# Optimization experiments

Measured on AMD Instinct MI355X. Metric: run time of the kernel, lower is better.

The kernel has to match this reference:

```python
import jax, jax.numpy as jnp
import numpy as np

B, L, D = 4, 1024, 512
H, DH = 8, 64
E = 65536  # total subgraph node entries
BN_EPS = 1e-5


def setup_inputs() -> dict:
    key = jax.random.key(0)
    ks = jax.random.split(key, 16)
    x = jax.random.normal(ks[0], (B, L, D), dtype=jnp.float32)
    lattice = jax.random.normal(ks[1], (B, 6), dtype=jnp.float32)  # unused (cond_dim=0)
    B_graph = jax.random.normal(ks[2], (B, L, L), dtype=jnp.float32) * 0.02
    N = B * L
    subgraph_node_index = jax.random.randint(ks[3], (E,), 0, N, dtype=jnp.int32)
    subgraph_indicator = jnp.sort(jax.random.randint(ks[4], (E,), 0, N, dtype=jnp.int32))
    attn_mask = jnp.triu(jnp.ones((L, L), dtype=bool), k=1)  # True = masked (causal)
    s = 0.02
    # Linear weights stored as [in, out]
    Wq = jax.random.normal(ks[5], (D, H * DH), jnp.float32) * s
    Wk = jax.random.normal(ks[6], (D, H * DH), jnp.float32) * s
    Wv = jax.random.normal(ks[7], (D, H * DH), jnp.float32) * s
    Wo = jax.random.normal(ks[8], (H * DH, D), jnp.float32) * s
    bq = jnp.zeros((H * DH,), jnp.float32)
    bk = jnp.zeros((H * DH,), jnp.float32)
    bv = jnp.zeros((H * DH,), jnp.float32)
    bo = jnp.zeros((D,), jnp.float32)
    Wmp = jax.random.normal(ks[9], (D, D), jnp.float32) * s
    bmp = jnp.zeros((D,), jnp.float32)
    bn_gamma = jnp.ones((2 * D,), jnp.float32)
    bn_beta = jnp.zeros((2 * D,), jnp.float32)
    Wex = jax.random.normal(ks[10], (2 * D, D), jnp.float32) * s
    bex = jnp.zeros((D,), jnp.float32)
    struct_scale = jnp.zeros((1,), jnp.float32) + 0.1  # nonzero so bias path is exercised
    return dict(x=x, lattice=lattice, B_graph=B_graph,
                subgraph_node_index=subgraph_node_index,
                subgraph_indicator=subgraph_indicator, attn_mask=attn_mask,
                Wq=Wq, bq=bq, Wk=Wk, bk=bk, Wv=Wv, bv=bv, Wo=Wo, bo=bo,
                Wmp=Wmp, bmp=bmp, bn_gamma=bn_gamma, bn_beta=bn_beta,
                Wex=Wex, bex=bex, struct_scale=struct_scale)


def _extractor(x_flat, sub_idx, sub_ind, Wmp, bmp, bn_gamma, bn_beta, Wex, bex):
    N = x_flat.shape[0]
    x_sub = x_flat[sub_idx]                       # [E, D]
    h = x_sub + (x_sub @ Wmp + bmp)               # 1 message-passing layer (residual)
    # scatter_mean over subgraph_indicator, dim_size=N
    sums = jax.ops.segment_sum(h, sub_ind, num_segments=N)
    cnt = jax.ops.segment_sum(jnp.ones((h.shape[0],), h.dtype), sub_ind, num_segments=N)
    h_pool = sums / jnp.maximum(cnt, 1.0)[:, None]
    out = jnp.concatenate([x_flat, h_pool], axis=-1)  # [N, 2D]
    # BatchNorm1d (training-mode batch stats)
    mu = jnp.mean(out, axis=0)
    var = jnp.var(out, axis=0)
    out = (out - mu) * jax.lax.rsqrt(var + BN_EPS) * bn_gamma + bn_beta
    return out @ Wex + bex                        # [N, D]


def reference(x, lattice, B_graph, subgraph_node_index, subgraph_indicator, attn_mask,
              Wq, bq, Wk, bk, Wv, bv, Wo, bo, Wmp, bmp, bn_gamma, bn_beta,
              Wex, bex, struct_scale):
    Bb, Ll, Dd = x.shape
    scale = 1.0 / np.sqrt(DH).astype(np.float32)
    q = (x @ Wq + bq).reshape(Bb, Ll, H, DH).transpose(0, 2, 1, 3)
    k = (x @ Wk + bk).reshape(Bb, Ll, H, DH).transpose(0, 2, 1, 3)
    v = (x @ Wv + bv).reshape(Bb, Ll, H, DH).transpose(0, 2, 1, 3)
    scores = jnp.einsum('bhqd,bhkd->bhqk', q, k) * scale
    # structural bias from GNN extractor
    x_flat = x.reshape(Bb * Ll, Dd)
    ex = _extractor(x_flat, subgraph_node_index, subgraph_indicator,
                    Wmp, bmp, bn_gamma, bn_beta, Wex, bex)
    x_struct = ex.reshape(Bb, Ll, Dd)
    K = jnp.einsum('bqd,bkd->bqk', x_struct, x_struct) / np.sqrt(Dd).astype(np.float32)
    scores = scores + struct_scale[0] * K[:, None]
    scores = scores + B_graph[:, None]
    mask = attn_mask[None, None]                  # (1,1,L,L), True = masked
    scores = jnp.where(mask, jnp.float32(-10000.0), scores)
    attn = jax.nn.softmax(scores.astype(jnp.float32), axis=-1).astype(scores.dtype)
    # dropout is identity (eval / p effectively 0)
    out = jnp.einsum('bhqk,bhkd->bhqd', attn, v)
    out = out.transpose(0, 2, 1, 3).reshape(Bb, Ll, H * DH)
    out = out @ Wo + bo
    return out, attn
```

## Files before the change

kernel.cpp:

```cpp
#include <hip/hip_runtime.h>
#include <math.h>

#define BB 4
#define LL 1024
#define DD 512
#define HH 8
#define DHH 64
#define EE 65536
#define NNODES 4096
#define HD 512
#define TWO_D 1024

typedef short bf16x8 __attribute__((ext_vector_type(8)));
typedef short short4v __attribute__((ext_vector_type(4)));
typedef float f32x4 __attribute__((ext_vector_type(4)));
typedef unsigned int u32;
#define GL_AS __attribute__((address_space(1)))
#define LDS_AS __attribute__((address_space(3)))

__device__ __forceinline__ short f2bf(float f) {
  u32 u = __builtin_bit_cast(u32, f);
  u = (u + 0x7fffu + ((u >> 16) & 1u)) >> 16;
  return (short)u;
}
__device__ __forceinline__ float b2f(short s) {
  u32 u = ((u32)(unsigned short)s) << 16;
  return __builtin_bit_cast(float, u);
}
__device__ __forceinline__ void gload_lds16(const short* g, short* l) {
  __builtin_amdgcn_global_load_lds((GL_AS const u32*)g, (LDS_AS u32*)l, 16, 0, 0);
}

template <int ROWS>
__device__ __forceinline__ void stage32(const short* g, int lda, short* lds, int tid) {
  const int w = tid >> 6, l = tid & 63;
#pragma unroll
  for (int rep = 0; rep < ROWS / 64; ++rep) {
    const int rbase = rep * 64 + w * 16;
    gload_lds16(g + (size_t)(rbase + (l >> 2)) * lda + (l & 3) * 8, lds + rbase * 32);
  }
}
__device__ __forceinline__ void stage64x128(const short* g, int lda, short* lds, int tid) {
  const int w = tid >> 6, l = tid & 63;
#pragma unroll
  for (int rep = 0; rep < 4; ++rep) {
    const int rbase = rep * 32 + w * 8;
    gload_lds16(g + (size_t)(rbase + (l >> 3)) * lda + (l & 7) * 8, lds + rbase * 64);
  }
}

template <int MREP, int NREP>
__device__ __forceinline__ void mfma_step(const short* As, const short* Bs, int lds_ld, int kofs,
                                          f32x4 (&acc)[MREP][NREP], int wr, int wc, int l) {
  bf16x8 a[MREP], b[NREP];
#pragma unroll
  for (int mi = 0; mi < MREP; ++mi) {
    const int row = wr * (MREP * 16) + mi * 16 + (l & 15);
    a[mi] = *(const bf16x8*)(As + row * lds_ld + kofs + ((l >> 4) << 3));
  }
#pragma unroll
  for (int ni = 0; ni < NREP; ++ni) {
    const int row = wc * (NREP * 16) + ni * 16 + (l & 15);
    b[ni] = *(const bf16x8*)(Bs + row * lds_ld + kofs + ((l >> 4) << 3));
  }
#pragma unroll
  for (int mi = 0; mi < MREP; ++mi)
#pragma unroll
    for (int ni = 0; ni < NREP; ++ni)
      acc[mi][ni] = __builtin_amdgcn_mfma_f32_16x16x32_bf16(a[mi], b[ni], acc[mi][ni], 0, 0, 0);
}

__global__ __launch_bounds__(256) void k_cast_x(const float* __restrict__ x, short* __restrict__ xb) {
  const int i = (blockIdx.x * 256 + threadIdx.x) * 8;
  float4 f0 = *(const float4*)(x + i), f1 = *(const float4*)(x + i + 4);
  bf16x8 s;
  s[0] = f2bf(f0.x); s[1] = f2bf(f0.y); s[2] = f2bf(f0.z); s[3] = f2bf(f0.w);
  s[4] = f2bf(f1.x); s[5] = f2bf(f1.y); s[6] = f2bf(f1.z); s[7] = f2bf(f1.w);
  *(bf16x8*)(xb + i) = s;
}

__global__ __launch_bounds__(256) void k_tcast(const float* __restrict__ W, short* __restrict__ out,
                                               int K, int N) {
  __shared__ float t[32][33];
  const int k0 = blockIdx.y * 32, n0 = blockIdx.x * 32;
  const int tx = threadIdx.x, ty = threadIdx.y;
#pragma unroll
  for (int i = 0; i < 4; ++i)
    t[ty + 8 * i][tx] = W[(size_t)(k0 + ty + 8 * i) * N + n0 + tx];
  __syncthreads();
#pragma unroll
  for (int i = 0; i < 4; ++i)
    out[(size_t)(n0 + ty + 8 * i) * K + k0 + tx] = f2bf(t[tx][ty + 8 * i]);
}

__global__ __launch_bounds__(256) void k_pack_bias(const float* bq, const float* bk,
                                                   const float* bv, const float* bmp,
                                                   float* __restrict__ bcat) {
  const int i = blockIdx.x * 256 + threadIdx.x;
  const float* src = (i < 512) ? bq : (i < 1024) ? bk : (i < 1536) ? bv : bmp;
  bcat[i] = src[i & 511];
}

__global__ __launch_bounds__(256) void k_gemm_qkvg(const short* __restrict__ A,
                                                   const short* __restrict__ Bw,
                                                   const float* __restrict__ bcat,
                                                   const float* __restrict__ x,
                                                   short* __restrict__ qT, short* __restrict__ kT,
                                                   short* __restrict__ vT, short* __restrict__ g_bf) {
  __shared__ __align__(16) short As[128 * 32];
  __shared__ __align__(16) short Bs[128 * 32];
  const int tid = threadIdx.x, l = tid & 63, w = tid >> 6, wr = w >> 1, wc = w & 1;
  const int m0 = blockIdx.y * 128, n0 = blockIdx.x * 128;
  f32x4 acc[4][4] = {};
  for (int k0 = 0; k0 < 512; k0 += 32) {
    stage32<128>(A + (size_t)m0 * 512 + k0, 512, As, tid);
    stage32<128>(Bw + (size_t)n0 * 512 + k0, 512, Bs, tid);
    __syncthreads();
    mfma_step<4, 4>(As, Bs, 32, 0, acc, wr, wc, l);
    __syncthreads();
  }
  const int lr = l >> 4, lc = l & 15;
#pragma unroll
  for (int mi = 0; mi < 4; ++mi)
#pragma unroll
    for (int ni = 0; ni < 4; ++ni) {
      const int col = n0 + wc * 64 + ni * 16 + lc;
      const int which = col >> 9;
#pragma unroll
      for (int r = 0; r < 4; ++r) {
        const int row = m0 + wr * 64 + mi * 16 + lr * 4 + r;
        float v = acc[mi][ni][r] + bcat[col];
        if (which < 3) {
          const int hh = (col >> 6) & 7, dh = col & 63;
          const int bb = row >> 10, ll2 = row & 1023;
          short* dst = (which == 0) ? qT : (which == 1) ? kT : vT;
          dst[((size_t)((bb * 8 + hh) * 1024 + ll2)) * 64 + dh] = f2bf(v);
        } else {
          const int c = col & 511;
          g_bf[(size_t)row * 512 + c] = f2bf(v + x[(size_t)row * 512 + c]);
        }
      }
    }
}

__global__ __launch_bounds__(256) void k_gemm_ex(const short* __restrict__ A,
                                                 const short* __restrict__ Bw,
                                                 const float* __restrict__ bias,
                                                 short* __restrict__ C) {
  __shared__ __align__(16) short As[64 * 32];
  __shared__ __align__(16) short Bs[128 * 32];
  const int tid = threadIdx.x, l = tid & 63, w = tid >> 6, wr = w >> 1, wc = w & 1;
  const int m0 = blockIdx.y * 64, n0 = blockIdx.x * 128;
  f32x4 acc[2][4] = {};
  for (int k0 = 0; k0 < 1024; k0 += 32) {
    stage32<64>(A + (size_t)m0 * 1024 + k0, 1024, As, tid);
    stage32<128>(Bw + (size_t)n0 * 1024 + k0, 1024, Bs, tid);
    __syncthreads();
    mfma_step<2, 4>(As, Bs, 32, 0, acc, wr, wc, l);
    __syncthreads();
  }
  const int lr = l >> 4, lc = l & 15;
#pragma unroll
  for (int mi = 0; mi < 2; ++mi)
#pragma unroll
    for (int ni = 0; ni < 4; ++ni) {
      const int col = n0 + wc * 64 + ni * 16 + lc;
      const float bv = bias[col];
#pragma unroll
      for (int r = 0; r < 4; ++r) {
        const int row = m0 + wr * 32 + mi * 16 + lr * 4 + r;
        C[(size_t)row * 512 + col] = f2bf(acc[mi][ni][r] + bv);
      }
    }
}

__global__ __launch_bounds__(256) void k_gemm_oproj(const short* __restrict__ A,
                                                    const short* __restrict__ Bw,
                                                    const float* __restrict__ bias,
                                                    float* __restrict__ C) {
  __shared__ __align__(16) short As[64 * 32];
  __shared__ __align__(16) short Bs[128 * 32];
  const int tid = threadIdx.x, l = tid & 63, w = tid >> 6, wr = w >> 1, wc = w & 1;
  const int m0 = blockIdx.y * 64, n0 = blockIdx.x * 128;
  f32x4 acc[2][4] = {};
  for (int k0 = 0; k0 < 512; k0 += 32) {
    stage32<64>(A + (size_t)m0 * 512 + k0, 512, As, tid);
    stage32<128>(Bw + (size_t)n0 * 512 + k0, 512, Bs, tid);
    __syncthreads();
    mfma_step<2, 4>(As, Bs, 32, 0, acc, wr, wc, l);
    __syncthreads();
  }
  const int lr = l >> 4, lc = l & 15;
#pragma unroll
  for (int mi = 0; mi < 2; ++mi)
#pragma unroll
    for (int ni = 0; ni < 4; ++ni) {
      const int col = n0 + wc * 64 + ni * 16 + lc;
      const float bv = bias[col];
#pragma unroll
      for (int r = 0; r < 4; ++r) {
        const int row = m0 + wr * 32 + mi * 16 + lr * 4 + r;
        C[(size_t)row * 512 + col] = acc[mi][ni][r] + bv;
      }
    }
}

__global__ __launch_bounds__(256) void k_kstruct(const short* __restrict__ ex,
                                                 const float* __restrict__ Bg,
                                                 const float* __restrict__ ssp,
                                                 float* __restrict__ Ksc) {
  const int mt = blockIdx.y, nt = blockIdx.x, b = blockIdx.z;
  if (nt > mt) return;
  __shared__ __align__(16) short As[128 * 32];
  __shared__ __align__(16) short Bs[128 * 32];
  const int tid = threadIdx.x, l = tid & 63, w = tid >> 6, wr = w >> 1, wc = w & 1;
  const int m0 = mt * 128, n0 = nt * 128;
  const short* Az = ex + (size_t)b * 1024 * 512;
  f32x4 acc[4][4] = {};
  for (int k0 = 0; k0 < 512; k0 += 32) {
    stage32<128>(Az + (size_t)m0 * 512 + k0, 512, As, tid);
    stage32<128>(Az + (size_t)n0 * 512 + k0, 512, Bs, tid);
    __syncthreads();
    mfma_step<4, 4>(As, Bs, 32, 0, acc, wr, wc, l);
    __syncthreads();
  }
  const float sc = ssp[0] * 0.04419417382415922f;
  const float* Bgb = Bg + (size_t)b * 1024 * 1024;
  float* Kb = Ksc + (size_t)b * 1024 * 1024;
  const int lr = l >> 4, lc = l & 15;
#pragma unroll
  for (int mi = 0; mi < 4; ++mi)
#pragma unroll
    for (int ni = 0; ni < 4; ++ni) {
      const int col = n0 + wc * 64 + ni * 16 + lc;
#pragma unroll
      for (int r = 0; r < 4; ++r) {
        const int row = m0 + wr * 64 + mi * 16 + lr * 4 + r;
        Kb[(size_t)row * 1024 + col] = fmaf(acc[mi][ni][r], sc, Bgb[(size_t)row * 1024 + col]);
      }
    }
}

__global__ __launch_bounds__(256) void k_scores(const short* __restrict__ qT,
                                                const short* __restrict__ kT,
                                                const float* __restrict__ Ksc,
                                                float* __restrict__ attn) {
  const int mt = blockIdx.y, nt = blockIdx.x, b = blockIdx.z;
  if (nt > mt) return;
  __shared__ __align__(16) short Qs[128 * 64];
  __shared__ __align__(16) short Ks_[128 * 64];
  const int tid = threadIdx.x, l = tid & 63, w = tid >> 6, wr = w >> 1, wc = w & 1;
  const int m0 = mt * 128, n0 = nt * 128;
  const int lr = l >> 4, lc = l & 15;
  const float* Kb = Ksc + (size_t)b * 1024 * 1024;
  for (int h = 0; h < 8; ++h) {
    const int z = b * 8 + h;
    stage64x128(qT + (size_t)z * 1024 * 64 + (size_t)m0 * 64, 64, Qs, tid);
    stage64x128(kT + (size_t)z * 1024 * 64 + (size_t)n0 * 64, 64, Ks_, tid);
    __syncthreads();
    f32x4 acc[4][4] = {};
    mfma_step<4, 4>(Qs, Ks_, 64, 0, acc, wr, wc, l);
    mfma_step<4, 4>(Qs, Ks_, 64, 32, acc, wr, wc, l);
    float* Az = attn + (size_t)z * 1024 * 1024;
#pragma unroll
    for (int mi = 0; mi < 4; ++mi)
#pragma unroll
      for (int ni = 0; ni < 4; ++ni) {
        const int col = n0 + wc * 64 + ni * 16 + lc;
#pragma unroll
        for (int r = 0; r < 4; ++r) {
          const int row = m0 + wr * 64 + mi * 16 + lr * 4 + r;
          Az[(size_t)row * 1024 + col] =
              fmaf(acc[mi][ni][r], 0.125f, Kb[(size_t)row * 1024 + col]);
        }
      }
    __syncthreads();
  }
}

__device__ __forceinline__ float block_sum(float v, float* red) {
#pragma unroll
  for (int o = 32; o > 0; o >>= 1) v += __shfl_down(v, o, 64);
  __syncthreads();
  if ((threadIdx.x & 63) == 0) red[threadIdx.x >> 6] = v;
  __syncthreads();
  return red[0] + red[1] + red[2] + red[3];
}
__device__ __forceinline__ float block_max(float v, float* red) {
#pragma unroll
  for (int o = 32; o > 0; o >>= 1) v = fmaxf(v, __shfl_down(v, o, 64));
  __syncthreads();
  if ((threadIdx.x & 63) == 0) red[threadIdx.x >> 6] = v;
  __syncthreads();
  return fmaxf(fmaxf(red[0], red[1]), fmaxf(red[2], red[3]));
}

__global__ __launch_bounds__(256) void k_softmax(float* __restrict__ attn) {
  __shared__ float buf[LL];
  __shared__ float red[4];
  const int i = blockIdx.x;
  float* row = attn + ((size_t)blockIdx.y * LL + i) * LL;
  const int jmax = i + 1;
  float mx = -INFINITY;
  for (int j = threadIdx.x; j < jmax; j += 256) {
    float v = row[j];
    buf[j] = v;
    mx = fmaxf(mx, v);
  }
  mx = block_max(mx, red);
  float sm = 0.f;
  for (int j = threadIdx.x; j < jmax; j += 256) {
    float e = expf(buf[j] - mx);
    buf[j] = e;
    sm += e;
  }
  sm = block_sum(sm, red);
  const float is = 1.0f / sm;
  for (int j = threadIdx.x; j < LL; j += 256)
    row[j] = (j < jmax) ? buf[j] * is : 0.0f;
}

__global__ __launch_bounds__(256) void k_pv(const float* __restrict__ attn,
                                            const short* __restrict__ vT,
                                            short* __restrict__ o_bf) {
  __shared__ __align__(16) short Pls[128 * 32];
  __shared__ __align__(16) short Vls[64 * 32];
  const int tid = threadIdx.x, l = tid & 63, w = tid >> 6;
  const int z = blockIdx.y, b = z >> 3, h = z & 7;
  const int m0 = blockIdx.x * 128;
  const float* Az = attn + (size_t)z * 1024 * 1024;
  const short* Vz = vT + (size_t)z * 1024 * 64;
  const int kend = m0 + 128;
  f32x4 acc[2][4] = {};
  const int pr = tid >> 1, jh = (tid & 1) * 16;
  const int vj = tid >> 3, vd0 = (tid & 7) * 8;
  for (int k0 = 0; k0 < kend; k0 += 32) {
    float tmpf[16];
    const float* src = Az + (size_t)(m0 + pr) * 1024 + k0 + jh;
#pragma unroll
    for (int c = 0; c < 4; ++c) *(float4*)(tmpf + c * 4) = *(const float4*)(src + c * 4);
    bf16x8 vv = *(const bf16x8*)(Vz + (size_t)(k0 + vj) * 64 + vd0);
    __syncthreads();
    bf16x8 s0, s1;
#pragma unroll
    for (int i = 0; i < 8; ++i) { s0[i] = f2bf(tmpf[i]); s1[i] = f2bf(tmpf[8 + i]); }
    *(bf16x8*)(Pls + pr * 32 + jh) = s0;
    *(bf16x8*)(Pls + pr * 32 + jh + 8) = s1;
#pragma unroll
    for (int i = 0; i < 8; ++i) Vls[(vd0 + i) * 32 + vj] = vv[i];
    __syncthreads();
    mfma_step<2, 4>(Pls, Vls, 32, 0, acc, w, 0, l);
  }
  const int lr = l >> 4, lc = l & 15;
#pragma unroll
  for (int mi = 0; mi < 2; ++mi)
#pragma unroll
    for (int ni = 0; ni < 4; ++ni)
#pragma unroll
      for (int r = 0; r < 4; ++r) {
        const int row = m0 + w * 32 + mi * 16 + lr * 4 + r;
        o_bf[((size_t)(b * 1024 + row)) * 512 + h * 64 + ni * 16 + lc] = f2bf(acc[mi][ni][r]);
      }
}

__global__ __launch_bounds__(128) void k_segmean(const short* __restrict__ g,
                                                 const int* __restrict__ idx,
                                                 const int* __restrict__ ind,
                                                 float* __restrict__ hp) {
  __shared__ int sh[2];
  const int s = blockIdx.x;
  if (threadIdx.x == 0) {
    int lo = 0, hi = EE;
    while (lo < hi) { int mid = (lo + hi) >> 1; if (ind[mid] < s) lo = mid + 1; else hi = mid; }
    sh[0] = lo;
    int lo2 = lo, hi2 = EE;
    while (lo2 < hi2) { int mid = (lo2 + hi2) >> 1; if (ind[mid] <= s) lo2 = mid + 1; else hi2 = mid; }
    sh[1] = lo2;
  }
  __syncthreads();
  const int lo = sh[0], hi = sh[1];
  const int d0 = threadIdx.x << 2;
  float a0 = 0.f, a1 = 0.f, a2 = 0.f, a3 = 0.f;
  for (int e = lo; e < hi; ++e) {
    const short4v v = *(const short4v*)(g + (size_t)idx[e] * 512 + d0);
    a0 += b2f(v[0]); a1 += b2f(v[1]); a2 += b2f(v[2]); a3 += b2f(v[3]);
  }
  const float ic = (hi > lo) ? 1.0f / (float)(hi - lo) : 0.0f;
  float4 o = {a0 * ic, a1 * ic, a2 * ic, a3 * ic};
  *(float4*)(hp + (size_t)s * 512 + d0) = o;
}

__global__ __launch_bounds__(256) void k_stats1(const float* __restrict__ x,
                                                const float* __restrict__ hp,
                                                float* __restrict__ scr) {
  const int blk = blockIdx.x, tid = threadIdx.x;
  const int c = tid * 2, r0 = blk * 128;
  float sx0 = 0, sx1 = 0, qx0 = 0, qx1 = 0, sh0 = 0, sh1 = 0, qh0 = 0, qh1 = 0;
  for (int r = 0; r < 128; ++r) {
    const size_t off = (size_t)(r0 + r) * 512 + c;
    float2 vx = *(const float2*)(x + off);
    float2 vh = *(const float2*)(hp + off);
    sx0 += vx.x; sx1 += vx.y; qx0 = fmaf(vx.x, vx.x, qx0); qx1 = fmaf(vx.y, vx.y, qx1);
    sh0 += vh.x; sh1 += vh.y; qh0 = fmaf(vh.x, vh.x, qh0); qh1 = fmaf(vh.y, vh.y, qh1);
  }
  float* p = scr + (size_t)blk * 4096;
  p[c] = sx0; p[c + 1] = sx1;
  p[512 + c] = sh0; p[512 + c + 1] = sh1;
  p[2048 + c] = qx0; p[2048 + c + 1] = qx1;
  p[2048 + 512 + c] = qh0; p[2048 + 512 + c + 1] = qh1;
}
__global__ __launch_bounds__(128) void k_stats2(const float* __restrict__ scr,
                                                float* __restrict__ mu, float* __restrict__ inv) {
  const int f = blockIdx.x * 128 + threadIdx.x;
  float s = 0.f, q = 0.f;
  for (int i = 0; i < 32; ++i) {
    s += scr[(size_t)i * 4096 + f];
    q += scr[(size_t)i * 4096 + 2048 + f];
  }
  const float m = s * (1.0f / NNODES);
  mu[f] = m;
  inv[f] = rsqrtf(q * (1.0f / NNODES) - m * m + 1e-5f);
}

__global__ __launch_bounds__(256) void k_norm(const float* __restrict__ x,
                                              const float* __restrict__ hp,
                                              const float* __restrict__ mu,
                                              const float* __restrict__ inv,
                                              const float* __restrict__ gamma,
                                              const float* __restrict__ beta,
                                              short* __restrict__ nrm) {
  const int gid = blockIdx.x * 256 + threadIdx.x;
  const int n = gid >> 8, f = (gid & 255) << 2;
  float4 v = (f < 512) ? *(const float4*)(x + (size_t)n * 512 + f)
                       : *(const float4*)(hp + (size_t)n * 512 + (f - 512));
  short4v o;
  o[0] = f2bf((v.x - mu[f + 0]) * inv[f + 0] * gamma[f + 0] + beta[f + 0]);
  o[1] = f2bf((v.y - mu[f + 1]) * inv[f + 1] * gamma[f + 1] + beta[f + 1]);
  o[2] = f2bf((v.z - mu[f + 2]) * inv[f + 2] * gamma[f + 2] + beta[f + 2]);
  o[3] = f2bf((v.w - mu[f + 3]) * inv[f + 3] * gamma[f + 3] + beta[f + 3]);
  *(short4v*)(nrm + (size_t)n * 1024 + f) = o;
}

extern "C" void kernel_launch(void* const* d_in, const int* in_sizes, int n_in,
                              void* d_out, int out_size, void* d_ws, size_t ws_size,
                              hipStream_t stream) {
  const float* x     = (const float*)d_in[0];
  const float* Bg    = (const float*)d_in[2];
  const int*   sidx  = (const int*)d_in[3];
  const int*   sind  = (const int*)d_in[4];
  const float* Wq    = (const float*)d_in[6];
  const float* bq    = (const float*)d_in[7];
  const float* Wk    = (const float*)d_in[8];
  const float* bk    = (const float*)d_in[9];
  const float* Wv    = (const float*)d_in[10];
  const float* bv    = (const float*)d_in[11];
  const float* Wo    = (const float*)d_in[12];
  const float* bo    = (const float*)d_in[13];
  const float* Wmp   = (const float*)d_in[14];
  const float* bmp   = (const float*)d_in[15];
  const float* gamma = (const float*)d_in[16];
  const float* beta  = (const float*)d_in[17];
  const float* Wex   = (const float*)d_in[18];
  const float* bex   = (const float*)d_in[19];
  const float* ssp   = (const float*)d_in[20];

  char* W = (char*)d_ws;
  short* x_bf  = (short*)(W + 0);
  short* WcatT = (short*)(W + 4194304);
  short* WexT  = (short*)(W + 6291456);
  short* WoT   = (short*)(W + 7340032);
  float* bcat  = (float*)(W + 7864320);
  short* qT    = (short*)(W + 7872512);
  short* kT    = (short*)(W + 12066816);
  short* vT    = (short*)(W + 16261120);
  short* g_bf  = (short*)(W + 20455424);
  float* hp    = (float*)(W + 24649728);
  short* nrm   = (short*)(W + 33038336);
  short* ex_bf = (short*)(W + 41426944);
  float* Ksc   = (float*)(W + 45621248);
  short* o_bf  = (short*)(W + 62398464);
  float* scr   = (float*)(W + 66592768);
  float* muv   = (float*)(W + 67117056);
  float* invv  = (float*)(W + 67121152);

  float* outp = (float*)d_out;
  float* attn = outp + (size_t)BB * LL * HD;

  dim3 t256(256), t32x8(32, 8);

  k_cast_x<<<dim3(1024), t256, 0, stream>>>(x, x_bf);
  k_tcast<<<dim3(16, 16), t32x8, 0, stream>>>(Wq,  WcatT,            512, 512);
  k_tcast<<<dim3(16, 16), t32x8, 0, stream>>>(Wk,  WcatT + 512*512,  512, 512);
  k_tcast<<<dim3(16, 16), t32x8, 0, stream>>>(Wv,  WcatT + 1024*512, 512, 512);
  k_tcast<<<dim3(16, 16), t32x8, 0, stream>>>(Wmp, WcatT + 1536*512, 512, 512);
  k_tcast<<<dim3(16, 32), t32x8, 0, stream>>>(Wex, WexT, 1024, 512);
  k_tcast<<<dim3(16, 16), t32x8, 0, stream>>>(Wo,  WoT,  512, 512);
  k_pack_bias<<<dim3(8), t256, 0, stream>>>(bq, bk, bv, bmp, bcat);

  k_gemm_qkvg<<<dim3(16, 32), t256, 0, stream>>>(x_bf, WcatT, bcat, x, qT, kT, vT, g_bf);

  k_segmean<<<dim3(NNODES), dim3(128), 0, stream>>>(g_bf, sidx, sind, hp);
  k_stats1<<<dim3(32), t256, 0, stream>>>(x, hp, scr);
  k_stats2<<<dim3(8), dim3(128), 0, stream>>>(scr, muv, invv);
  k_norm<<<dim3(4096), t256, 0, stream>>>(x, hp, muv, invv, gamma, beta, nrm);
  k_gemm_ex<<<dim3(4, 64), t256, 0, stream>>>(nrm, WexT, bex, ex_bf);

  k_kstruct<<<dim3(8, 8, 4), t256, 0, stream>>>(ex_bf, Bg, ssp, Ksc);

  k_scores<<<dim3(8, 8, 4), t256, 0, stream>>>(qT, kT, Ksc, attn);
  k_softmax<<<dim3(1024, 32), t256, 0, stream>>>(attn);
  k_pv<<<dim3(8, 32), t256, 0, stream>>>(attn, vT, o_bf);

  k_gemm_oproj<<<dim3(4, 64), t256, 0, stream>>>(o_bf, WoT, bo, outp);
}
```

Before: 408.7 us.

## Fuse scores, softmax and PV into one two-pass flash-style attention kernel

```diff
diff --git a/kernel.cpp b/kernel.cpp
--- a/kernel.cpp
+++ b/kernel.cpp
@@ -40,14 +40,6 @@
     gload_lds16(g + (size_t)(rbase + (l >> 2)) * lda + (l & 3) * 8, lds + rbase * 32);
   }
 }
-__device__ __forceinline__ void stage64x128(const short* g, int lda, short* lds, int tid) {
-  const int w = tid >> 6, l = tid & 63;
-#pragma unroll
-  for (int rep = 0; rep < 4; ++rep) {
-    const int rbase = rep * 32 + w * 8;
-    gload_lds16(g + (size_t)(rbase + (l >> 3)) * lda + (l & 7) * 8, lds + rbase * 64);
-  }
-}
 
 template <int MREP, int NREP>
 __device__ __forceinline__ void mfma_step(const short* As, const short* Bs, int lds_ld, int kofs,
@@ -68,6 +60,12 @@
 #pragma unroll
     for (int ni = 0; ni < NREP; ++ni)
       acc[mi][ni] = __builtin_amdgcn_mfma_f32_16x16x32_bf16(a[mi], b[ni], acc[mi][ni], 0, 0, 0);
+}
+
+template <int ROWB>
+__device__ __forceinline__ bf16x8 ldsw(const short* base, int row, int bir) {
+  const int bo = (row * ROWB + bir) ^ ((row & 7) << 4);
+  return *(const bf16x8*)((const char*)base + bo);
 }
 
 __global__ __launch_bounds__(256) void k_cast_x(const float* __restrict__ x, short* __restrict__ xb) {
@@ -77,6 +75,25 @@
   s[0] = f2bf(f0.x); s[1] = f2bf(f0.y); s[2] = f2bf(f0.z); s[3] = f2bf(f0.w);
   s[4] = f2bf(f1.x); s[5] = f2bf(f1.y); s[6] = f2bf(f1.z); s[7] = f2bf(f1.w);
   *(bf16x8*)(xb + i) = s;
+}
+
+__global__ __launch_bounds__(256) void k_tcast5(const float* __restrict__ Wq, const float* __restrict__ Wk,
+                                                const float* __restrict__ Wv, const float* __restrict__ Wmp,
+                                                const float* __restrict__ Wo,
+                                                short* __restrict__ WcatT, short* __restrict__ WoT) {
+  __shared__ float t[32][33];
+  const int zz = blockIdx.z;
+  const float* W = (zz == 0) ? Wq : (zz == 1) ? Wk : (zz == 2) ? Wv : (zz == 3) ? Wmp : Wo;
+  short* out = (zz < 4) ? (WcatT + zz * 512 * 512) : WoT;
+  const int k0 = blockIdx.y * 32, n0 = blockIdx.x * 32;
+  const int tx = threadIdx.x, ty = threadIdx.y;
+#pragma unroll
+  for (int i = 0; i < 4; ++i)
+    t[ty + 8 * i][tx] = W[(size_t)(k0 + ty + 8 * i) * 512 + n0 + tx];
+  __syncthreads();
+#pragma unroll
+  for (int i = 0; i < 4; ++i)
+    out[(size_t)(n0 + ty + 8 * i) * 512 + k0 + tx] = f2bf(t[tx][ty + 8 * i]);
 }
 
 __global__ __launch_bounds__(256) void k_tcast(const float* __restrict__ W, short* __restrict__ out,
@@ -241,126 +258,226 @@
     }
 }
 
-__global__ __launch_bounds__(256) void k_scores(const short* __restrict__ qT,
-                                                const short* __restrict__ kT,
-                                                const float* __restrict__ Ksc,
-                                                float* __restrict__ attn) {
-  const int mt = blockIdx.y, nt = blockIdx.x, b = blockIdx.z;
-  if (nt > mt) return;
-  __shared__ __align__(16) short Qs[128 * 64];
-  __shared__ __align__(16) short Ks_[128 * 64];
-  const int tid = threadIdx.x, l = tid & 63, w = tid >> 6, wr = w >> 1, wc = w & 1;
-  const int m0 = mt * 128, n0 = nt * 128;
-  const int lr = l >> 4, lc = l & 15;
-  const float* Kb = Ksc + (size_t)b * 1024 * 1024;
-  for (int h = 0; h < 8; ++h) {
-    const int z = b * 8 + h;
-    stage64x128(qT + (size_t)z * 1024 * 64 + (size_t)m0 * 64, 64, Qs, tid);
-    stage64x128(kT + (size_t)z * 1024 * 64 + (size_t)n0 * 64, 64, Ks_, tid);
-    __syncthreads();
-    f32x4 acc[4][4] = {};
-    mfma_step<4, 4>(Qs, Ks_, 64, 0, acc, wr, wc, l);
-    mfma_step<4, 4>(Qs, Ks_, 64, 32, acc, wr, wc, l);
-    float* Az = attn + (size_t)z * 1024 * 1024;
-#pragma unroll
-    for (int mi = 0; mi < 4; ++mi)
+__global__ __launch_bounds__(256) void k_attn(const short* __restrict__ qT,
+                                              const short* __restrict__ kT,
+                                              const short* __restrict__ vT,
+                                              const float* __restrict__ Ksc,
+                                              float* __restrict__ attn,
+                                              short* __restrict__ o_bf) {
+  __shared__ __align__(16) short Qs[64 * 64];
+  __shared__ __align__(16) short Ks[128 * 64];
+  __shared__ __align__(16) short Ps[64 * 128];
+  __shared__ __align__(16) short Vls[64 * 128];
+  __shared__ float mred[2][64], sred[2][64];
+
+  const int tid = threadIdx.x, l = tid & 63, w = tid >> 6;
+  const int wr = w >> 1, wc = w & 1, lr = l >> 4, lc = l & 15;
+  const int z = blockIdx.y, b = z >> 3, h = z & 7;
+  const int mt = (z & 16) ? (15 - (int)blockIdx.x) : (int)blockIdx.x;
+  const int r0 = mt * 64;
+  const int NT = (mt + 2) >> 1;
+
+  const short* Qz = qT + (size_t)z * 65536 + (size_t)r0 * 64;
+  const short* Kz = kT + (size_t)z * 65536;
+  const short* Vz = vT + (size_t)z * 65536;
+  const float* Kb = Ksc + (size_t)b * 1048576 + (size_t)r0 * 1024;
+  float* Az = attn + (size_t)z * 1048576 + (size_t)r0 * 1024;
+
+#pragma unroll
+  for (int rep = 0; rep < 2; ++rep) {
+    const int rbase = w * 16 + rep * 8;
+    gload_lds16(Qz + (size_t)(rbase + (l >> 3)) * 64 + ((l & 7) ^ (l >> 3)) * 8,
+                Qs + rbase * 64);
+  }
+
+  const int zc0 = NT * 128;
+  if (zc0 < 1024) {
+    const int cw = (1024 - zc0) >> 2;
+    for (int idx = tid; idx < 64 * cw; idx += 256) {
+      const int rowi = idx / cw, c4 = idx - rowi * cw;
+      float4 zf = {0.f, 0.f, 0.f, 0.f};
+      *(float4*)&Az[(size_t)rowi * 1024 + zc0 + (c4 << 2)] = zf;
+    }
+  }
+
+  float m8[8], s8[8];
+#pragma unroll
+  for (int i = 0; i < 8; ++i) { m8[i] = -INFINITY; s8[i] = 0.f; }
+
+  for (int nt = 0; nt < NT; ++nt) {
+    const int n0 = nt * 128;
+    __syncthreads();
+#pragma unroll
+    for (int rep = 0; rep < 4; ++rep) {
+      const int rbase = rep * 32 + w * 8;
+      gload_lds16(Kz + (size_t)(n0 + rbase + (l >> 3)) * 64 + ((l & 7) ^ (l >> 3)) * 8,
+                  Ks + rbase * 64);
+    }
+    __syncthreads();
+    f32x4 acc[2][4] = {};
+#pragma unroll
+    for (int kk = 0; kk < 2; ++kk) {
+      const int bir = kk * 64 + lr * 16;
+      bf16x8 a[2], bb[4];
+#pragma unroll
+      for (int mi = 0; mi < 2; ++mi) a[mi] = ldsw<128>(Qs, wr * 32 + mi * 16 + lc, bir);
+#pragma unroll
+      for (int ni = 0; ni < 4; ++ni) bb[ni] = ldsw<128>(Ks, wc * 64 + ni * 16 + lc, bir);
+#pragma unroll
+      for (int mi = 0; mi < 2; ++mi)
+#pragma unroll
+        for (int ni = 0; ni < 4; ++ni)
+          acc[mi][ni] = __builtin_amdgcn_mfma_f32_16x16x32_bf16(a[mi], bb[ni], acc[mi][ni], 0, 0, 0);
+    }
+    const bool lastT = (nt == NT - 1);
+#pragma unroll
+    for (int mi = 0; mi < 2; ++mi)
+#pragma unroll
+      for (int rr = 0; rr < 4; ++rr) {
+        const int row = wr * 32 + mi * 16 + lr * 4 + rr;
+        const int slot = mi * 4 + rr;
+        float vals[4], tm = -INFINITY;
+#pragma unroll
+        for (int ni = 0; ni < 4; ++ni) {
+          const int col = wc * 64 + ni * 16 + lc;
+          float sc = fmaf(acc[mi][ni][rr], 0.125f, Kb[(size_t)row * 1024 + n0 + col]);
+          if (lastT && (n0 + col > r0 + row)) sc = -INFINITY;
+          vals[ni] = sc;
+          tm = fmaxf(tm, sc);
+        }
+        if (tm > -INFINITY) {
+          const float mn = fmaxf(m8[slot], tm);
+          float ts = 0.f;
+#pragma unroll
+          for (int ni = 0; ni < 4; ++ni) ts += expf(vals[ni] - mn);
+          s8[slot] = s8[slot] * expf(m8[slot] - mn) + ts;
+          m8[slot] = mn;
+        }
+      }
+  }
+
+#pragma unroll
+  for (int off = 1; off < 16; off <<= 1)
+#pragma unroll
+    for (int i = 0; i < 8; ++i) {
+      const float mo = __shfl_xor(m8[i], off, 64);
+      const float so = __shfl_xor(s8[i], off, 64);
+      const float mn = fmaxf(m8[i], mo);
+      if (mn > -INFINITY)
+        s8[i] = s8[i] * expf(m8[i] - mn) + so * expf(mo - mn);
+      m8[i] = mn;
+    }
+  if (lc == 0) {
+#pragma unroll
+    for (int mi = 0; mi < 2; ++mi)
+#pragma unroll
+      for (int rr = 0; rr < 4; ++rr) {
+        const int row = wr * 32 + mi * 16 + lr * 4 + rr;
+        mred[wc][row] = m8[mi * 4 + rr];
+        sred[wc][row] = s8[mi * 4 + rr];
+      }
+  }
+  __syncthreads();
+  float mf[8], inv_s[8];
+#pragma unroll
+  for (int mi = 0; mi < 2; ++mi)
+#pragma unroll
+    for (int rr = 0; rr < 4; ++rr) {
+      const int row = wr * 32 + mi * 16 + lr * 4 + rr;
+      const float ma = mred[0][row], mb = mred[1][row];
+      const float mF = fmaxf(ma, mb);
+      const float sF = sred[0][row] * expf(ma - mF) + sred[1][row] * expf(mb - mF);
+      mf[mi * 4 + rr] = mF;
+      inv_s[mi * 4 + rr] = 1.0f / sF;
+    }
+
+  f32x4 oacc[4];
+#pragma unroll
+  for (int i = 0; i < 4; ++i) oacc[i] = f32x4{0.f, 0.f, 0.f, 0.f};
+
+  for (int nt = 0; nt < NT; ++nt) {
+    const int n0 = nt * 128;
+    __syncthreads();
+#pragma unroll
+    for (int rep = 0; rep < 4; ++rep) {
+      const int rbase = rep * 32 + w * 8;
+      gload_lds16(Kz + (size_t)(n0 + rbase + (l >> 3)) * 64 + ((l & 7) ^ (l >> 3)) * 8,
+                  Ks + rbase * 64);
+    }
+    {
+      const int j = tid >> 1, d0 = (tid & 1) * 32;
+      const short* vsrc = Vz + (size_t)(n0 + j) * 64 + d0;
+      bf16x8 v0 = *(const bf16x8*)(vsrc);
+      bf16x8 v1 = *(const bf16x8*)(vsrc + 8);
+      bf16x8 v2 = *(const bf16x8*)(vsrc + 16);
+      bf16x8 v3 = *(const bf16x8*)(vsrc + 24);
+#pragma unroll
+      for (int i = 0; i < 8; ++i) {
+        int dh = d0 + i;
+        *(short*)((char*)Vls + ((dh * 256 + j * 2) ^ ((dh & 7) << 4))) = v0[i];
+        dh = d0 + 8 + i;
+        *(short*)((char*)Vls + ((dh * 256 + j * 2) ^ ((dh & 7) << 4))) = v1[i];
+        dh = d0 + 16 + i;
+        *(short*)((char*)Vls + ((dh * 256 + j * 2) ^ ((dh & 7) << 4))) = v2[i];
+        dh = d0 + 24 + i;
+        *(short*)((char*)Vls + ((dh * 256 + j * 2) ^ ((dh & 7) << 4))) = v3[i];
+      }
+    }
+    __syncthreads();
+    f32x4 acc[2][4] = {};
+#pragma unroll
+    for (int kk = 0; kk < 2; ++kk) {
+      const int bir = kk * 64 + lr * 16;
+      bf16x8 a[2], bb[4];
+#pragma unroll
+      for (int mi = 0; mi < 2; ++mi) a[mi] = ldsw<128>(Qs, wr * 32 + mi * 16 + lc, bir);
+#pragma unroll
+      for (int ni = 0; ni < 4; ++ni) bb[ni] = ldsw<128>(Ks, wc * 64 + ni * 16 + lc, bir);
+#pragma unroll
+      for (int mi = 0; mi < 2; ++mi)
+#pragma unroll
+        for (int ni = 0; ni < 4; ++ni)
+          acc[mi][ni] = __builtin_amdgcn_mfma_f32_16x16x32_bf16(a[mi], bb[ni], acc[mi][ni], 0, 0, 0);
+    }
+    const bool lastT = (nt == NT - 1);
+#pragma unroll
+    for (int mi = 0; mi < 2; ++mi)
+#pragma unroll
+      for (int rr = 0; rr < 4; ++rr) {
+        const int row = wr * 32 + mi * 16 + lr * 4 + rr;
+        const int slot = mi * 4 + rr;
+#pragma unroll
+        for (int ni = 0; ni < 4; ++ni) {
+          const int col = wc * 64 + ni * 16 + lc;
+          const float sc = fmaf(acc[mi][ni][rr], 0.125f, Kb[(size_t)row * 1024 + n0 + col]);
+          float p = 0.f;
+          if (!(lastT && (n0 + col > r0 + row)))
+            p = expf(sc - mf[slot]) * inv_s[slot];
+          Az[(size_t)row * 1024 + n0 + col] = p;
+          *(short*)((char*)Ps + ((row * 256 + col * 2) ^ ((row & 7) << 4))) = f2bf(p);
+        }
+      }
+    __syncthreads();
+#pragma unroll
+    for (int ks = 0; ks < 4; ++ks) {
+      const int bir = ks * 64 + lr * 16;
+      bf16x8 a = ldsw<256>(Ps, w * 16 + lc, bir);
 #pragma unroll
       for (int ni = 0; ni < 4; ++ni) {
-        const int col = n0 + wc * 64 + ni * 16 + lc;
-#pragma unroll
-        for (int r = 0; r < 4; ++r) {
-          const int row = m0 + wr * 64 + mi * 16 + lr * 4 + r;
-          Az[(size_t)row * 1024 + col] =
-              fmaf(acc[mi][ni][r], 0.125f, Kb[(size_t)row * 1024 + col]);
-        }
-      }
-    __syncthreads();
-  }
-}
-
-__device__ __forceinline__ float block_sum(float v, float* red) {
-#pragma unroll
-  for (int o = 32; o > 0; o >>= 1) v += __shfl_down(v, o, 64);
-  __syncthreads();
-  if ((threadIdx.x & 63) == 0) red[threadIdx.x >> 6] = v;
-  __syncthreads();
-  return red[0] + red[1] + red[2] + red[3];
-}
-__device__ __forceinline__ float block_max(float v, float* red) {
-#pragma unroll
-  for (int o = 32; o > 0; o >>= 1) v = fmaxf(v, __shfl_down(v, o, 64));
-  __syncthreads();
-  if ((threadIdx.x & 63) == 0) red[threadIdx.x >> 6] = v;
-  __syncthreads();
-  return fmaxf(fmaxf(red[0], red[1]), fmaxf(red[2], red[3]));
-}
-
-__global__ __launch_bounds__(256) void k_softmax(float* __restrict__ attn) {
-  __shared__ float buf[LL];
-  __shared__ float red[4];
-  const int i = blockIdx.x;
-  float* row = attn + ((size_t)blockIdx.y * LL + i) * LL;
-  const int jmax = i + 1;
-  float mx = -INFINITY;
-  for (int j = threadIdx.x; j < jmax; j += 256) {
-    float v = row[j];
-    buf[j] = v;
-    mx = fmaxf(mx, v);
-  }
-  mx = block_max(mx, red);
-  float sm = 0.f;
-  for (int j = threadIdx.x; j < jmax; j += 256) {
-    float e = expf(buf[j] - mx);
-    buf[j] = e;
-    sm += e;
-  }
-  sm = block_sum(sm, red);
-  const float is = 1.0f / sm;
-  for (int j = threadIdx.x; j < LL; j += 256)
-    row[j] = (j < jmax) ? buf[j] * is : 0.0f;
-}
-
-__global__ __launch_bounds__(256) void k_pv(const float* __restrict__ attn,
-                                            const short* __restrict__ vT,
-                                            short* __restrict__ o_bf) {
-  __shared__ __align__(16) short Pls[128 * 32];
-  __shared__ __align__(16) short Vls[64 * 32];
-  const int tid = threadIdx.x, l = tid & 63, w = tid >> 6;
-  const int z = blockIdx.y, b = z >> 3, h = z & 7;
-  const int m0 = blockIdx.x * 128;
-  const float* Az = attn + (size_t)z * 1024 * 1024;
-  const short* Vz = vT + (size_t)z * 1024 * 64;
-  const int kend = m0 + 128;
-  f32x4 acc[2][4] = {};
-  const int pr = tid >> 1, jh = (tid & 1) * 16;
-  const int vj = tid >> 3, vd0 = (tid & 7) * 8;
-  for (int k0 = 0; k0 < kend; k0 += 32) {
-    float tmpf[16];
-    const float* src = Az + (size_t)(m0 + pr) * 1024 + k0 + jh;
-#pragma unroll
-    for (int c = 0; c < 4; ++c) *(float4*)(tmpf + c * 4) = *(const float4*)(src + c * 4);
-    bf16x8 vv = *(const bf16x8*)(Vz + (size_t)(k0 + vj) * 64 + vd0);
-    __syncthreads();
-    bf16x8 s0, s1;
-#pragma unroll
-    for (int i = 0; i < 8; ++i) { s0[i] = f2bf(tmpf[i]); s1[i] = f2bf(tmpf[8 + i]); }
-    *(bf16x8*)(Pls + pr * 32 + jh) = s0;
-    *(bf16x8*)(Pls + pr * 32 + jh + 8) = s1;
-#pragma unroll
-    for (int i = 0; i < 8; ++i) Vls[(vd0 + i) * 32 + vj] = vv[i];
-    __syncthreads();
-    mfma_step<2, 4>(Pls, Vls, 32, 0, acc, w, 0, l);
-  }
-  const int lr = l >> 4, lc = l & 15;
-#pragma unroll
-  for (int mi = 0; mi < 2; ++mi)
-#pragma unroll
-    for (int ni = 0; ni < 4; ++ni)
-#pragma unroll
-      for (int r = 0; r < 4; ++r) {
-        const int row = m0 + w * 32 + mi * 16 + lr * 4 + r;
-        o_bf[((size_t)(b * 1024 + row)) * 512 + h * 64 + ni * 16 + lc] = f2bf(acc[mi][ni][r]);
-      }
+        bf16x8 bb = ldsw<256>(Vls, ni * 16 + lc, bir);
+        oacc[ni] = __builtin_amdgcn_mfma_f32_16x16x32_bf16(a, bb, oacc[ni], 0, 0, 0);
+      }
+    }
+  }
+
+#pragma unroll
+  for (int ni = 0; ni < 4; ++ni)
+#pragma unroll
+    for (int rr = 0; rr < 4; ++rr) {
+      const int row = r0 + w * 16 + lr * 4 + rr;
+      const int dh = ni * 16 + lc;
+      o_bf[((size_t)(b * 1024 + row)) * 512 + h * 64 + dh] = f2bf(oacc[ni][rr]);
+    }
 }
 
 __global__ __launch_bounds__(128) void k_segmean(const short* __restrict__ g,
@@ -489,12 +606,8 @@
   dim3 t256(256), t32x8(32, 8);
 
   k_cast_x<<<dim3(1024), t256, 0, stream>>>(x, x_bf);
-  k_tcast<<<dim3(16, 16), t32x8, 0, stream>>>(Wq,  WcatT,            512, 512);
-  k_tcast<<<dim3(16, 16), t32x8, 0, stream>>>(Wk,  WcatT + 512*512,  512, 512);
-  k_tcast<<<dim3(16, 16), t32x8, 0, stream>>>(Wv,  WcatT + 1024*512, 512, 512);
-  k_tcast<<<dim3(16, 16), t32x8, 0, stream>>>(Wmp, WcatT + 1536*512, 512, 512);
+  k_tcast5<<<dim3(16, 16, 5), t32x8, 0, stream>>>(Wq, Wk, Wv, Wmp, Wo, WcatT, WoT);
   k_tcast<<<dim3(16, 32), t32x8, 0, stream>>>(Wex, WexT, 1024, 512);
-  k_tcast<<<dim3(16, 16), t32x8, 0, stream>>>(Wo,  WoT,  512, 512);
   k_pack_bias<<<dim3(8), t256, 0, stream>>>(bq, bk, bv, bmp, bcat);
 
   k_gemm_qkvg<<<dim3(16, 32), t256, 0, stream>>>(x_bf, WcatT, bcat, x, qT, kT, vT, g_bf);
@@ -507,9 +620,7 @@
 
   k_kstruct<<<dim3(8, 8, 4), t256, 0, stream>>>(ex_bf, Bg, ssp, Ksc);
 
-  k_scores<<<dim3(8, 8, 4), t256, 0, stream>>>(qT, kT, Ksc, attn);
-  k_softmax<<<dim3(1024, 32), t256, 0, stream>>>(attn);
-  k_pv<<<dim3(8, 32), t256, 0, stream>>>(attn, vT, o_bf);
+  k_attn<<<dim3(16, 32), t256, 0, stream>>>(qT, kT, vT, Ksc, attn, o_bf);
 
   k_gemm_oproj<<<dim3(4, 64), t256, 0, stream>>>(o_bf, WoT, bo, outp);
 }
```

After: 421.8 us. +3.2%, slower.
